# Kernel optimization log

Measured on AMD Instinct MI355X. Metric: run time of the kernel, lower is better.

The kernel has to match this reference:

```python
import jax, jax.numpy as jnp
import numpy as np

B, S, D, H = 2, 2048, 1024, 16
HD = D // H
SCALING = HD ** -0.5


def _length_mask(lengths, seqlen):
    return (jnp.arange(seqlen)[None, :] < jnp.asarray(lengths)[:, None]).astype(jnp.int32)


def setup_inputs() -> dict:
    key = jax.random.key(0)
    ks = jax.random.split(key, 10)
    std = D ** -0.5
    inp = {
        "hidden_states": jax.random.normal(ks[0], (B, S, D), dtype=jnp.float32),
        "Wq": jax.random.normal(ks[1], (D, D), dtype=jnp.float32) * std,
        "bq": jax.random.normal(ks[2], (D,), dtype=jnp.float32) * 0.02,
        "Wk": jax.random.normal(ks[3], (D, D), dtype=jnp.float32) * std,
        "bk": jax.random.normal(ks[4], (D,), dtype=jnp.float32) * 0.02,
        "Wv": jax.random.normal(ks[5], (D, D), dtype=jnp.float32) * std,
        "bv": jax.random.normal(ks[6], (D,), dtype=jnp.float32) * 0.02,
        "Wo": jax.random.normal(ks[7], (D, D), dtype=jnp.float32) * std,
        "bo": jax.random.normal(ks[8], (D,), dtype=jnp.float32) * 0.02,
        # variable valid lengths per batch element (padding at the end)
        "query_mask_1d": _length_mask([S, S - 512], S),
        "key_mask_1d": _length_mask([S, S - 512], S),
    }
    return inp


def reference(hidden_states, Wq, bq, Wk, bk, Wv, bv, Wo, bo, query_mask_1d, key_mask_1d):
    bsz, tgt_len, _ = hidden_states.shape
    # projections (dropout p=0 / eval -> identity)
    q = (hidden_states @ Wq + bq) * SCALING
    k = hidden_states @ Wk + bk
    v = hidden_states @ Wv + bv
    q = q.reshape(bsz, tgt_len, H, HD).transpose(0, 2, 1, 3)  # [B,H,S,HD]
    k = k.reshape(bsz, -1, H, HD).transpose(0, 2, 1, 3)
    v = v.reshape(bsz, -1, H, HD).transpose(0, 2, 1, 3)

    scores = jnp.einsum("bhqd,bhkd->bhqk", q, k)  # [B,H,S,S]
    q_valid = (query_mask_1d != 0)[:, None, :, None]  # [B,1,S,1]
    k_valid = (key_mask_1d != 0)[:, None, None, :]    # [B,1,1,S]
    # masked_fill(-inf) on padded keys; padded-query rows would be all -inf ->
    # softmax NaN -> nan_to_num(0). We compute the same result NaN-free by
    # zeroing the scores of padded-query rows and zeroing their probs after.
    s = jnp.where(k_valid, scores, -jnp.inf)
    s = jnp.where(q_valid, s, 0.0)
    attn_weights = jax.nn.softmax(s, axis=-1) * q_valid  # == softmax + nan_to_num

    attn_output = jnp.einsum("bhqk,bhkd->bhqd", attn_weights, v)
    attn_output = attn_output.transpose(0, 2, 1, 3).reshape(bsz, tgt_len, D)
    attn_output = attn_output @ Wo + bo
    return attn_output
```

## Files before the change

### kernel.cpp

```cpp
#include <hip/hip_runtime.h>
#include <stdint.h>

#define BB 2
#define SS 2048
#define DD 1024
#define HH 16
#define HDIM 64
#define MTOT (BB*SS)
#define QK_SCALE_LOG2E 0.180336880f

typedef unsigned short u16;
typedef __attribute__((ext_vector_type(8))) __bf16 bf16x8;
typedef __attribute__((ext_vector_type(4))) float f32x4;

static __device__ __forceinline__ float exp2_hw(float x) {
    return __builtin_amdgcn_exp2f(x);
}

static __device__ __forceinline__ u16 f2bu(float f) {
    union { float f; uint32_t u; } c; c.f = f;
    uint32_t u = c.u + 0x7fffu + ((c.u >> 16) & 1u);
    return (u16)(u >> 16);
}

static __device__ __forceinline__ u16 f2b_hw(float f) {
    __bf16 b = (__bf16)f;
    union { __bf16 b; u16 u; } c; c.b = b;
    return c.u;
}

static __device__ __forceinline__ uint32_t cvt_pk_bf16(float lo, float hi) {
    uint32_t r;
    asm("v_cvt_pk_bf16_f32 %0, %1, %2" : "=v"(r) : "v"(lo), "v"(hi));
    return r;
}

static __device__ __forceinline__ void gload_lds16(const void* g, void* l) {
    __builtin_amdgcn_global_load_lds(
        (const __attribute__((address_space(1))) uint32_t*)(g),
        (__attribute__((address_space(3))) uint32_t*)(l),
        16, 0, 0);
}

__global__ void k_prep(const float* __restrict__ x, u16* __restrict__ xb,
                       const float* __restrict__ Wq, const float* __restrict__ Wk,
                       const float* __restrict__ Wv, const float* __restrict__ Wo,
                       u16* __restrict__ Wqkv_t, u16* __restrict__ Wo_t) {
    const int which = blockIdx.z;
    if (which == 4) {
        const int tid = (blockIdx.y * 32 + blockIdx.x) * 256 + threadIdx.y * 32 + threadIdx.x;
        #pragma unroll
        for (int r = 0; r < 4; ++r) {
            const int i = (tid + r * 262144) * 4;
            float4 v = *(const float4*)(x + i);
            ushort4 o;
            o.x = f2bu(v.x); o.y = f2bu(v.y); o.z = f2bu(v.z); o.w = f2bu(v.w);
            *(ushort4*)(xb + i) = o;
        }
        return;
    }
    __shared__ float tile[32][33];
    const float* W = (which == 0) ? Wq : (which == 1) ? Wk : (which == 2) ? Wv : Wo;
    u16* dst = (which < 3) ? (Wqkv_t + (size_t)which * DD * DD) : Wo_t;
    const int n0 = blockIdx.x * 32, k0 = blockIdx.y * 32;
    const int tx = threadIdx.x, ty = threadIdx.y;
    #pragma unroll
    for (int i = 0; i < 32; i += 8)
        tile[ty + i][tx] = W[(size_t)(k0 + ty + i) * DD + (n0 + tx)];
    __syncthreads();
    #pragma unroll
    for (int i = 0; i < 32; i += 8)
        dst[(size_t)(n0 + ty + i) * DD + (k0 + tx)] = f2bu(tile[tx][ty + i]);
}

#define PH(AP, Q, READB, STAGECODE, TAILWAIT)                                 \
  { bf16x8 afr[2][2];                                                         \
    _Pragma("unroll") for (int m2 = 0; m2 < 2; ++m2)                          \
      _Pragma("unroll") for (int ks = 0; ks < 2; ++ks)                        \
        afr[m2][ks] = rdA(AP, 2*(Q)+m2, ks);                                  \
    if (READB) {                                                              \
      _Pragma("unroll") for (int nf = 0; nf < 3; ++nf)                        \
        _Pragma("unroll") for (int ks = 0; ks < 2; ++ks)                      \
          bfr[nf][ks] = rdB(BP_, nf, ks);                                     \
    }                                                                         \
    STAGECODE;                                                                \
    __builtin_amdgcn_s_barrier();                                             \
    asm volatile("s_waitcnt lgkmcnt(0)" ::: "memory");                        \
    __builtin_amdgcn_sched_barrier(0);                                        \
    __builtin_amdgcn_s_setprio(1);                                            \
    _Pragma("unroll") for (int m2 = 0; m2 < 2; ++m2)                          \
      _Pragma("unroll") for (int nf = 0; nf < 3; ++nf)                        \
        _Pragma("unroll") for (int ks = 0; ks < 2; ++ks)                      \
          acc[2*(Q)+m2][nf] = __builtin_amdgcn_mfma_f32_16x16x32_bf16(        \
              afr[m2][ks], bfr[nf][ks], acc[2*(Q)+m2][nf], 0, 0, 0);          \
    __builtin_amdgcn_s_setprio(0);                                            \
    TAILWAIT;                                                                 \
    __builtin_amdgcn_s_barrier();                                             \
  }

__global__ __launch_bounds__(512, 2) void k_gemm_qkv(
    const u16* __restrict__ Xb, const u16* __restrict__ Wt,
    const float* __restrict__ bq, const float* __restrict__ bk_, const float* __restrict__ bv,
    u16* __restrict__ Qb, u16* __restrict__ Kb, u16* __restrict__ Vt)
{
    __shared__ u16 AsA[3][256 * 64];
    __shared__ u16 BsB[2][192 * 64];

    const int flat = blockIdx.y * 16 + blockIdx.x;
    const int xcd = flat & 7, idx = flat >> 3;
    const int by = ((xcd >> 1) << 2) + (idx >> 3);
    const int bx = ((xcd & 1) << 3) + (idx & 7);
    const int m0 = by << 8, n0 = bx * 192;

    const int t = threadIdx.x;
    const int lane = t & 63, w = t >> 6;
    const int wm = (w >> 2) << 7, wn = (w & 3) * 48;
    const int lr = lane & 15, lg = lane >> 4;

    const u16* Asrc = Xb + (size_t)m0 * DD;
    const u16* Bsrc = Wt + (size_t)n0 * DD;

    f32x4 acc[8][3] = {};
    bf16x8 bfr[3][2];

    auto stgA = [&](u16* bufp, int half, int tt) {
        #pragma unroll
        for (int r = 0; r < 2; ++r) {
            int off = (t + (r << 9)) << 4;
            int row = off >> 7, colb = off & 127;
            int scol = colb ^ ((row & 7) << 4);
            gload_lds16(Asrc + (size_t)((half << 7) + row) * DD + (tt << 6) + (scol >> 1),
                        (char*)bufp + (half << 14) + off);
        }
    };
    auto stgB = [&](u16* bufp, int tt) {
        #pragma unroll
        for (int r = 0; r < 3; ++r) {
            int off = (t + (r << 9)) << 4;
            int row = off >> 7, colb = off & 127;
            int scol = colb ^ ((row & 7) << 4);
            gload_lds16(Bsrc + (size_t)row * DD + (tt << 6) + (scol >> 1),
                        (char*)bufp + off);
        }
    };

    auto rdA = [&](const u16* bufp, int mf, int ks) {
        const int row = wm + (mf << 4) + lr;
        const int col = ((ks << 6) + (lg << 4)) ^ ((row & 7) << 4);
        return *(const bf16x8*)((const char*)bufp + row * 128 + col);
    };
    auto rdB = [&](const u16* bufp, int nf, int ks) {
        const int row = wn + (nf << 4) + lr;
        const int col = ((ks << 6) + (lg << 4)) ^ ((row & 7) << 4);
        return *(const bf16x8*)((const char*)bufp + row * 128 + col);
    };

    u16* pE = AsA[0]; u16* pO = AsA[1]; u16* pS = AsA[2];
    u16* Bs0 = BsB[0]; u16* Bs1 = BsB[1];

    stgA(pE, 0, 0); stgA(pE, 1, 0); stgB(Bs0, 0);
    stgA(pO, 0, 1); stgA(pO, 1, 1); stgB(Bs1, 1);
    asm volatile("s_waitcnt vmcnt(7)" ::: "memory");
    __builtin_amdgcn_sched_barrier(0);
    __builtin_amdgcn_s_barrier();

    #pragma unroll 1
    for (int j = 0; j < 7; ++j) {
        const int tb = 2 * j;
        { const u16* BP_ = Bs0;
          PH(pE, 0, true,  { stgA(pS, 0, tb + 2); }, {});
          PH(pE, 1, false, { stgA(pS, 1, tb + 2); }, {});
          PH(pE, 2, false, { stgB(Bs0, tb + 2); }, {});
          PH(pE, 3, false, {},
             { asm volatile("s_waitcnt vmcnt(7)" ::: "memory"); }); }
        { const u16* BP_ = Bs1;
          PH(pO, 0, true,  { stgA(pE, 0, tb + 3); }, {});
          PH(pO, 1, false, { stgA(pE, 1, tb + 3); }, {});
          PH(pO, 2, false, { stgB(Bs1, tb + 3); }, {});
          PH(pO, 3, false, {},
             { asm volatile("s_waitcnt vmcnt(7)" ::: "memory"); }); }
        u16* oE = pE; u16* oO = pO; u16* oS = pS;
        pE = oS; pO = oE; pS = oO;
    }
    { const u16* BP_ = Bs0;
      PH(pE, 0, true,  {}, {});
      PH(pE, 1, false, {}, {});
      PH(pE, 2, false, {}, {});
      PH(pE, 3, false, {},
         { asm volatile("s_waitcnt vmcnt(0)" ::: "memory"); }); }
    { const u16* BP_ = Bs1;
      PH(pO, 0, true,  {}, {});
      PH(pO, 1, false, {}, {});
      PH(pO, 2, false, {}, {});
      PH(pO, 3, false, {}, {}); }

    #pragma unroll
    for (int mf = 0; mf < 8; ++mf) {
        #pragma unroll
        for (int nf = 0; nf < 3; ++nf) {
            const int n = n0 + wn + (nf << 4) + lr;
            const int mbase = m0 + wm + (mf << 4) + (lg << 2);
            const int b_ = mbase >> 11;
            const int s_ = mbase & 2047;
            const int seg = n >> 10;
            const int nn = n & 1023;
            const int hh = nn >> 6, d = nn & 63;
            if (seg == 0) {
                const float bias = bq[nn];
                u16* dstp = Qb + (((size_t)b_ * HH + hh) * SS + s_) * HDIM + d;
                #pragma unroll
                for (int r = 0; r < 4; ++r)
                    dstp[(size_t)r * HDIM] = f2bu((acc[mf][nf][r] + bias) * QK_SCALE_LOG2E);
            } else if (seg == 1) {
                const float bias = bk_[nn];
                u16* dstp = Kb + (((size_t)b_ * HH + hh) * SS + s_) * HDIM + d;
                #pragma unroll
                for (int r = 0; r < 4; ++r)
                    dstp[(size_t)r * HDIM] = f2bu(acc[mf][nf][r] + bias);
            } else {
                const float bias = bv[nn];
                ushort4 pk;
                pk.x = f2bu(acc[mf][nf][0] + bias);
                pk.y = f2bu(acc[mf][nf][1] + bias);
                pk.z = f2bu(acc[mf][nf][2] + bias);
                pk.w = f2bu(acc[mf][nf][3] + bias);
                *(ushort4*)(Vt + (((size_t)b_ * HH + hh) * HDIM + d) * SS + s_) = pk;
            }
        }
    }
}

__global__ __launch_bounds__(512, 4) void k_attn(
    const u16* __restrict__ Qb, const u16* __restrict__ Kb, const u16* __restrict__ Vt,
    const int* __restrict__ qmask, const int* __restrict__ kmask,
    u16* __restrict__ X2)
{
    const int i = blockIdx.x;
    const int xcd = i & 7, j = i >> 3;
    const int qt = j & 15;
    const int bh = xcd + ((j >> 4) << 3);
    const int b_ = bh >> 4;
    const int h = bh & 15;

    const int t = threadIdx.x;
    const int lane = t & 63, w = t >> 6;
    const int lr = lane & 15, lg = lane >> 4;

    __shared__ u16 Ks[3][64 * 64];
    __shared__ u16 Vs[3][64 * 64];

    const int q0 = qt << 7;
    const size_t bhs = (size_t)b_ * HH + h;
    const u16* Qbase = Qb + bhs * SS * HDIM;
    const char* KbaseB = (const char*)(Kb + bhs * SS * HDIM);
    const char* VbaseB = (const char*)(Vt + bhs * HDIM * SS);

    if (qmask[b_ * SS + q0] == 0) {
        #pragma unroll
        for (int r = 0; r < 4; ++r) {
            const int q = q0 + (w << 4) + (lg << 2) + r;
            #pragma unroll
            for (int nf = 0; nf < 4; ++nf)
                X2[((size_t)b_ * SS + q) * DD + (h << 6) + (nf << 4) + lr] = 0;
        }
        return;
    }

    int kv = (lane < 32) ? kmask[b_ * SS + (lane << 6)] : 0;
    unsigned long long bal = __ballot(kv != 0);
    const int nkt = __popcll(bal);

    bf16x8 qf[2];
    #pragma unroll
    for (int ks = 0; ks < 2; ++ks)
        qf[ks] = *(const bf16x8*)(Qbase + (size_t)(q0 + (w << 4) + lr) * HDIM + (ks << 5) + (lg << 3));

    bf16x8 vones;
    #pragma unroll
    for (int i2 = 0; i2 < 8; ++i2) vones[i2] = (__bf16)1.0f;

    f32x4 o[4] = {};
    f32x4 lacc = {};

    auto stage = [&](int buf, int kb) {
        const int off = t << 4;
        const int row = off >> 7, colb = off & 127;
        const int scol = colb ^ ((row & 7) << 4);
        gload_lds16(KbaseB + (size_t)(kb + row) * 128 + scol, (char*)Ks[buf] + off);
        gload_lds16(VbaseB + ((size_t)row * SS + (size_t)kb) * 2 + scol, (char*)Vs[buf] + off);
    };

    if (nkt > 0) stage(0, 0);
    if (nkt > 1) stage(1, 64);
    if (nkt > 1) { asm volatile("s_waitcnt vmcnt(2)" ::: "memory"); }
    else         { asm volatile("s_waitcnt vmcnt(0)" ::: "memory"); }
    __builtin_amdgcn_sched_barrier(0);
    __builtin_amdgcn_s_barrier();

    int cur = 0;
    #pragma unroll 1
    for (int kt = 0; kt < nkt; ++kt) {
        const int kb = kt << 6;
        const int nxt = (cur == 2) ? 0 : cur + 1;
        const int nx2 = (nxt == 2) ? 0 : nxt + 1;
        if (kt + 2 < nkt) stage(nx2, kb + 128);

        f32x4 sf[4] = {};
        __builtin_amdgcn_s_setprio(1);
        #pragma unroll
        for (int ks = 0; ks < 2; ++ks) {
            #pragma unroll
            for (int f = 0; f < 4; ++f) {
                const int krow = (f << 4) + lr;
                const int kcol = ((ks << 6) + (lg << 4)) ^ ((krow & 7) << 4);
                bf16x8 kf = *(const bf16x8*)((const char*)Ks[cur] + krow * 128 + kcol);
                sf[f] = __builtin_amdgcn_mfma_f32_16x16x32_bf16(kf, qf[ks], sf[f], 0, 0, 0);
            }
        }
        __builtin_amdgcn_s_setprio(0);
        if (kt == nkt - 1) {
            #pragma unroll
            for (int f = 0; f < 4; ++f) {
                #pragma unroll
                for (int r = 0; r < 4; ++r) {
                    if (kmask[b_ * SS + kb + (f << 4) + (lg << 2) + r] == 0)
                        sf[f][r] = -1e30f;
                }
            }
        }
        #pragma unroll
        for (int f = 0; f < 4; ++f)
            #pragma unroll
            for (int r = 0; r < 4; ++r)
                sf[f][r] = exp2_hw(sf[f][r]);

        uint32_t wv[4][2];
        #pragma unroll
        for (int f = 0; f < 4; ++f) {
            wv[f][0] = cvt_pk_bf16(sf[f][0], sf[f][1]);
            wv[f][1] = cvt_pk_bf16(sf[f][2], sf[f][3]);
        }
        bf16x8 pa[2];
        #pragma unroll
        for (int ks2 = 0; ks2 < 2; ++ks2) {
            uint32_t u0, u1, u2, u3;
            {
                uint32_t A = wv[2 * ks2][0], B = wv[2 * ks2 + 1][0];
                asm("v_permlane32_swap_b32 %0, %1" : "+v"(A), "+v"(B));
                asm("v_permlane16_swap_b32 %0, %1" : "+v"(A), "+v"(B));
                u0 = A; u2 = B;
            }
            {
                uint32_t A = wv[2 * ks2][1], B = wv[2 * ks2 + 1][1];
                asm("v_permlane32_swap_b32 %0, %1" : "+v"(A), "+v"(B));
                asm("v_permlane16_swap_b32 %0, %1" : "+v"(A), "+v"(B));
                u1 = A; u3 = B;
            }
            union { uint32_t q[4]; bf16x8 v; } cv;
            cv.q[0] = u0; cv.q[1] = u1; cv.q[2] = u2; cv.q[3] = u3;
            pa[ks2] = cv.v;
        }

        __builtin_amdgcn_s_setprio(1);
        #pragma unroll
        for (int ks = 0; ks < 2; ++ks) {
            lacc = __builtin_amdgcn_mfma_f32_16x16x32_bf16(pa[ks], vones, lacc, 0, 0, 0);
            #pragma unroll
            for (int nf = 0; nf < 4; ++nf) {
                const int vrow = (nf << 4) + lr;
                const int vcol = ((ks << 6) + (lg << 4)) ^ ((vrow & 7) << 4);
                bf16x8 vb = *(const bf16x8*)((const char*)Vs[cur] + vrow * 128 + vcol);
                o[nf] = __builtin_amdgcn_mfma_f32_16x16x32_bf16(pa[ks], vb, o[nf], 0, 0, 0);
            }
        }
        __builtin_amdgcn_s_setprio(0);

        if (kt + 2 < nkt) { asm volatile("s_waitcnt vmcnt(2)" ::: "memory"); }
        else              { asm volatile("s_waitcnt vmcnt(0)" ::: "memory"); }
        __builtin_amdgcn_sched_barrier(0);
        __builtin_amdgcn_s_barrier();
        cur = nxt;
    }

    #pragma unroll
    for (int r = 0; r < 4; ++r) {
        const int q = q0 + (w << 4) + (lg << 2) + r;
        float l = lacc[r];
        float inv = (l > 0.f) ? __builtin_amdgcn_rcpf(l) : 0.f;
        if (qmask[b_ * SS + q] == 0) inv = 0.f;
        #pragma unroll
        for (int nf = 0; nf < 4; ++nf)
            X2[((size_t)b_ * SS + q) * DD + (h << 6) + (nf << 4) + lr] = f2b_hw(o[nf][r] * inv);
    }
}

__global__ __launch_bounds__(256) void k_gemm_out(
    const u16* __restrict__ X2, const u16* __restrict__ Wot,
    const float* __restrict__ bo, float* __restrict__ out)
{
    __shared__ u16 As2[2][128 * 64];
    __shared__ u16 Bs2[2][128 * 64];
    const int flat = blockIdx.y * 8 + blockIdx.x;
    const int xcd = flat & 7, idx = flat >> 3;
    const int by = (xcd << 2) + (idx >> 3);
    const int bx = idx & 7;
    const int m0 = by * 128, n0 = bx * 128;
    const int t = threadIdx.x;
    const int lane = t & 63, w = t >> 6;
    const int wm = (w >> 1) << 6, wn = (w & 1) << 6;
    const int lr = lane & 15, lg = lane >> 4;

    f32x4 acc[4][4] = {};

    auto stage = [&](int buf, int k0) {
        #pragma unroll
        for (int i = 0; i < 4; ++i) {
            int off = (t + (i << 8)) << 4;
            int row = off >> 7, colb = off & 127;
            int scol = colb ^ ((row & 7) << 4);
            gload_lds16(X2 + (size_t)(m0 + row) * DD + k0 + (scol >> 1), (char*)As2[buf] + off);
            gload_lds16(Wot + (size_t)(n0 + row) * DD + k0 + (scol >> 1), (char*)Bs2[buf] + off);
        }
    };

    stage(0, 0);
    __syncthreads();

    int cur = 0;
    for (int kt = 0; kt < 16; ++kt) {
        if (kt < 15) stage(cur ^ 1, (kt + 1) << 6);
        #pragma unroll
        for (int ks = 0; ks < 2; ++ks) {
            bf16x8 a[4], b[4];
            #pragma unroll
            for (int i = 0; i < 4; ++i) {
                const int row = wm + (i << 4) + lr;
                a[i] = *(const bf16x8*)((const char*)As2[cur] + row * 128 + (((ks << 6) + (lg << 4)) ^ ((row & 7) << 4)));
            }
            #pragma unroll
            for (int i = 0; i < 4; ++i) {
                const int row = wn + (i << 4) + lr;
                b[i] = *(const bf16x8*)((const char*)Bs2[cur] + row * 128 + (((ks << 6) + (lg << 4)) ^ ((row & 7) << 4)));
            }
            #pragma unroll
            for (int mi = 0; mi < 4; ++mi)
                #pragma unroll
                for (int ni = 0; ni < 4; ++ni)
                    acc[mi][ni] = __builtin_amdgcn_mfma_f32_16x16x32_bf16(a[mi], b[ni], acc[mi][ni], 0, 0, 0);
        }
        __syncthreads();
        cur ^= 1;
    }

    #pragma unroll
    for (int mi = 0; mi < 4; ++mi) {
        #pragma unroll
        for (int ni = 0; ni < 4; ++ni) {
            const int n = n0 + wn + (ni << 4) + lr;
            const int mbase = m0 + wm + (mi << 4) + (lg << 2);
            const float bias = bo[n];
            #pragma unroll
            for (int r = 0; r < 4; ++r)
                out[(size_t)(mbase + r) * DD + n] = acc[mi][ni][r] + bias;
        }
    }
}

extern "C" void kernel_launch(void* const* d_in, const int* in_sizes, int n_in,
                              void* d_out, int out_size, void* d_ws, size_t ws_size,
                              hipStream_t stream) {
    const float* hs = (const float*)d_in[0];
    const float* Wq = (const float*)d_in[1];
    const float* bq = (const float*)d_in[2];
    const float* Wk = (const float*)d_in[3];
    const float* bk = (const float*)d_in[4];
    const float* Wv = (const float*)d_in[5];
    const float* bv = (const float*)d_in[6];
    const float* Wo = (const float*)d_in[7];
    const float* bo = (const float*)d_in[8];
    const int* qm = (const int*)d_in[9];
    const int* km = (const int*)d_in[10];
    float* out = (float*)d_out;

    char* ws = (char*)d_ws;
    const size_t MB = 1024 * 1024;
    u16* Xb  = (u16*)(ws + 0);
    u16* Wt3 = (u16*)(ws + 8 * MB);
    u16* Wot = (u16*)(ws + 14 * MB);
    u16* Qb  = (u16*)(ws + 16 * MB);
    u16* Kb  = (u16*)(ws + 24 * MB);
    u16* Vt  = (u16*)(ws + 32 * MB);
    u16* X2  = (u16*)(ws + 40 * MB);

    k_prep<<<dim3(32, 32, 5), dim3(32, 8), 0, stream>>>(hs, Xb, Wq, Wk, Wv, Wo, Wt3, Wot);
    k_gemm_qkv<<<dim3(16, 16), dim3(512), 0, stream>>>(Xb, Wt3, bq, bk, bv, Qb, Kb, Vt);
    k_attn<<<dim3(512), dim3(512), 0, stream>>>(Qb, Kb, Vt, qm, km, X2);
    k_gemm_out<<<dim3(8, 32), dim3(256), 0, stream>>>(X2, Wot, bo, out);
}
```

Before: 107.1 us.

## Double-buffer LDS fragment reads in QKV GEMM to overlap with MFMA

Restructures the QKV projection GEMM main loop so that the A/B register fragments for the next phase are loaded from shared memory while the current phase's MFMAs execute, using ping-pong register buffers. It drops the explicit lgkmcnt(0) wait before each MFMA block and moves the global-load vmcnt waits earlier so the next tile's B fragments can be read ahead. This aims to hide LDS read latency behind matrix math, at the cost of more live VGPRs. It also relies on the compiler inserting the correct LDS waits now that the explicit one is gone.

```diff
diff --git a/kernel.cpp b/kernel.cpp
--- a/kernel.cpp
+++ b/kernel.cpp
@@ -73,28 +73,21 @@
         dst[(size_t)(n0 + ty + i) * DD + (k0 + tx)] = f2bu(tile[tx][ty + i]);
 }
 
-#define PH(AP, Q, READB, STAGECODE, TAILWAIT)                                 \
-  { bf16x8 afr[2][2];                                                         \
-    _Pragma("unroll") for (int m2 = 0; m2 < 2; ++m2)                          \
-      _Pragma("unroll") for (int ks = 0; ks < 2; ++ks)                        \
-        afr[m2][ks] = rdA(AP, 2*(Q)+m2, ks);                                  \
-    if (READB) {                                                              \
-      _Pragma("unroll") for (int nf = 0; nf < 3; ++nf)                        \
-        _Pragma("unroll") for (int ks = 0; ks < 2; ++ks)                      \
-          bfr[nf][ks] = rdB(BP_, nf, ks);                                     \
-    }                                                                         \
+#define VMH(N) do { asm volatile("s_waitcnt vmcnt(" #N ")" ::: "memory"); \
+                    __builtin_amdgcn_sched_barrier(0); } while (0)
+
+#define PHX(AFRC, BFRC, MFQ, RDNEXT, STAGECODE)                               \
+  { RDNEXT;                                                                   \
     STAGECODE;                                                                \
     __builtin_amdgcn_s_barrier();                                             \
-    asm volatile("s_waitcnt lgkmcnt(0)" ::: "memory");                        \
     __builtin_amdgcn_sched_barrier(0);                                        \
     __builtin_amdgcn_s_setprio(1);                                            \
     _Pragma("unroll") for (int m2 = 0; m2 < 2; ++m2)                          \
       _Pragma("unroll") for (int nf = 0; nf < 3; ++nf)                        \
         _Pragma("unroll") for (int ks = 0; ks < 2; ++ks)                      \
-          acc[2*(Q)+m2][nf] = __builtin_amdgcn_mfma_f32_16x16x32_bf16(        \
-              afr[m2][ks], bfr[nf][ks], acc[2*(Q)+m2][nf], 0, 0, 0);          \
+          acc[2*(MFQ)+m2][nf] = __builtin_amdgcn_mfma_f32_16x16x32_bf16(      \
+              AFRC[m2][ks], BFRC[nf][ks], acc[2*(MFQ)+m2][nf], 0, 0, 0);      \
     __builtin_amdgcn_s_setprio(0);                                            \
-    TAILWAIT;                                                                 \
     __builtin_amdgcn_s_barrier();                                             \
   }
 
@@ -121,7 +114,8 @@
     const u16* Bsrc = Wt + (size_t)n0 * DD;
 
     f32x4 acc[8][3] = {};
-    bf16x8 bfr[3][2];
+    bf16x8 afr0[2][2], afr1[2][2];
+    bf16x8 bfr0[3][2], bfr1[3][2];
 
     auto stgA = [&](u16* bufp, int half, int tt) {
         #pragma unroll
@@ -154,6 +148,20 @@
         const int col = ((ks << 6) + (lg << 4)) ^ ((row & 7) << 4);
         return *(const bf16x8*)((const char*)bufp + row * 128 + col);
     };
+    auto rdAq = [&](bf16x8 (&dst)[2][2], const u16* bufp, int q) {
+        #pragma unroll
+        for (int m2 = 0; m2 < 2; ++m2)
+            #pragma unroll
+            for (int ks = 0; ks < 2; ++ks)
+                dst[m2][ks] = rdA(bufp, 2 * q + m2, ks);
+    };
+    auto rdBt = [&](bf16x8 (&dst)[3][2], const u16* bufp) {
+        #pragma unroll
+        for (int nf = 0; nf < 3; ++nf)
+            #pragma unroll
+            for (int ks = 0; ks < 2; ++ks)
+                dst[nf][ks] = rdB(bufp, nf, ks);
+    };
 
     u16* pE = AsA[0]; u16* pO = AsA[1]; u16* pS = AsA[2];
     u16* Bs0 = BsB[0]; u16* Bs1 = BsB[1];
@@ -163,36 +171,34 @@
     asm volatile("s_waitcnt vmcnt(7)" ::: "memory");
     __builtin_amdgcn_sched_barrier(0);
     __builtin_amdgcn_s_barrier();
+    rdAq(afr0, pE, 0);
+    rdBt(bfr0, Bs0);
 
     #pragma unroll 1
     for (int j = 0; j < 7; ++j) {
         const int tb = 2 * j;
-        { const u16* BP_ = Bs0;
-          PH(pE, 0, true,  { stgA(pS, 0, tb + 2); }, {});
-          PH(pE, 1, false, { stgA(pS, 1, tb + 2); }, {});
-          PH(pE, 2, false, { stgB(Bs0, tb + 2); }, {});
-          PH(pE, 3, false, {},
-             { asm volatile("s_waitcnt vmcnt(7)" ::: "memory"); }); }
-        { const u16* BP_ = Bs1;
-          PH(pO, 0, true,  { stgA(pE, 0, tb + 3); }, {});
-          PH(pO, 1, false, { stgA(pE, 1, tb + 3); }, {});
-          PH(pO, 2, false, { stgB(Bs1, tb + 3); }, {});
-          PH(pO, 3, false, {},
-             { asm volatile("s_waitcnt vmcnt(7)" ::: "memory"); }); }
+        PHX(afr0, bfr0, 0, { rdAq(afr1, pE, 1); }, { stgA(pS, 0, tb + 2); });
+        PHX(afr1, bfr0, 1, { rdAq(afr0, pE, 2); }, { stgA(pS, 1, tb + 2); });
+        PHX(afr0, bfr0, 2, { rdAq(afr1, pE, 3); }, { stgB(Bs0, tb + 2); });
+        VMH(7);
+        PHX(afr1, bfr0, 3, { rdAq(afr0, pO, 0); rdBt(bfr1, Bs1); }, {});
+        PHX(afr0, bfr1, 0, { rdAq(afr1, pO, 1); }, { stgA(pE, 0, tb + 3); });
+        PHX(afr1, bfr1, 1, { rdAq(afr0, pO, 2); }, { stgA(pE, 1, tb + 3); });
+        PHX(afr0, bfr1, 2, { rdAq(afr1, pO, 3); }, { stgB(Bs1, tb + 3); });
+        VMH(7);
+        PHX(afr1, bfr1, 3, { rdAq(afr0, pS, 0); rdBt(bfr0, Bs0); }, {});
         u16* oE = pE; u16* oO = pO; u16* oS = pS;
         pE = oS; pO = oE; pS = oO;
     }
-    { const u16* BP_ = Bs0;
-      PH(pE, 0, true,  {}, {});
-      PH(pE, 1, false, {}, {});
-      PH(pE, 2, false, {}, {});
-      PH(pE, 3, false, {},
-         { asm volatile("s_waitcnt vmcnt(0)" ::: "memory"); }); }
-    { const u16* BP_ = Bs1;
-      PH(pO, 0, true,  {}, {});
-      PH(pO, 1, false, {}, {});
-      PH(pO, 2, false, {}, {});
-      PH(pO, 3, false, {}, {}); }
+    PHX(afr0, bfr0, 0, { rdAq(afr1, pE, 1); }, {});
+    PHX(afr1, bfr0, 1, { rdAq(afr0, pE, 2); }, {});
+    PHX(afr0, bfr0, 2, { rdAq(afr1, pE, 3); }, {});
+    VMH(0);
+    PHX(afr1, bfr0, 3, { rdAq(afr0, pO, 0); rdBt(bfr1, Bs1); }, {});
+    PHX(afr0, bfr1, 0, { rdAq(afr1, pO, 1); }, {});
+    PHX(afr1, bfr1, 1, { rdAq(afr0, pO, 2); }, {});
+    PHX(afr0, bfr1, 2, { rdAq(afr1, pO, 3); }, {});
+    PHX(afr1, bfr1, 3, {}, {});
 
     #pragma unroll
     for (int mf = 0; mf < 8; ++mf) {
```

Result: no change. 106.7 us (-0.4%).
